# Kernel optimization log

Hardware: AMD Instinct MI355X
Metric: run time of the kernel (lower is better)

Reference implementation:

```python
import jax, jax.numpy as jnp
import numpy as np

N = 4096       # num_nodes (must equal out_features: final div broadcasts [C,N]/[N,1])
IN_F = 1024    # module in_features
OUT_F = 4096   # module out_features == N
F_RAW = 512    # raw node feature dim fed to the in-forward Linear


def setup_inputs() -> dict:
    key = jax.random.key(0)
    ks = jax.random.split(key, 5)
    node_features = jax.random.normal(ks[0], (N, F_RAW), dtype=jnp.float32)
    adjacency_matrix = jax.random.bernoulli(ks[1], 0.004, (N, N)).astype(jnp.float32)
    eye = jnp.eye(N, dtype=jnp.float32)
    A0 = adjacency_matrix * (1.0 - eye)                 # adjacency w/o self loops
    S = (A0 @ A0 + A0) * (1.0 - eye)                    # sibling matrix, zero diag
    mask_hadamard = S[:, None, :]                       # [N,1,N]
    mask_father = adjacency_matrix[:, None, :]          # [N,1,N]
    neighbor_count = jnp.maximum(A0.sum(axis=1, keepdims=True), 1.0)  # [N,1]
    lim = float(1.0 / np.sqrt(F_RAW))
    linear_w = jax.random.uniform(ks[2], (IN_F, F_RAW), minval=-lim, maxval=lim, dtype=jnp.float32)
    linear_b = jax.random.uniform(ks[3], (IN_F,), minval=-lim, maxval=lim, dtype=jnp.float32)
    weight = jax.random.normal(ks[4], (IN_F, OUT_F), dtype=jnp.float32) * float(np.sqrt(2.0 / IN_F))
    return dict(node_features=node_features, adjacency_matrix=adjacency_matrix,
                mask_father=mask_father, neighbor_count=neighbor_count,
                mask_hadamard=mask_hadamard, linear_w=linear_w, linear_b=linear_b,
                weight=weight)


def reference(node_features, adjacency_matrix, mask_father, neighbor_count,
              mask_hadamard, linear_w, linear_b, weight):
    # Linear + projection: wf[n,c]
    x = node_features @ linear_w.T + linear_b           # [N, IN_F]
    wf = x @ weight                                      # [N, C]
    # Original builds masked_hadamard[j,i,c] = wf[i,c]*wf[j,c]*S[i,j] ([N,C,N]),
    # contracts with adjacency over i, masks with adj[k,j], sums over k:
    #   sum_hadamard[c,j] = wf[j,c] * sum_i (sum_k adj[k,j]*adj[k,i]) * S[i,j] * wf[i,c]
    # Fused form avoids the O(N^2 C) intermediates; same math.
    A_out = mask_father[:, 0, :]                         # adj[k,j]  [N,N]
    S = mask_hadamard[:, 0, :]                           # S[i,j]    [N,N]
    G = A_out.T @ adjacency_matrix                       # G[j,i] = sum_k adj[k,j]*adj[k,i]
    P = G * S.T                                          # P[j,i] = G[j,i]*S[i,j]
    sum_hadamard = (wf * (P @ wf)).T                     # [C, N]
    # Final broadcast division exactly as torch: [C,N] / [N,1] (requires C==N)
    return sum_hadamard / jnp.square(neighbor_count)
```

## Files before the change

kernel.cpp:

```cpp
#include <hip/hip_runtime.h>
#include <hip/hip_bf16.h>

typedef __attribute__((ext_vector_type(8))) short s16x8;
typedef __attribute__((ext_vector_type(4))) float f32x4;
typedef __attribute__((ext_vector_type(8))) unsigned short u16x8;

__device__ __forceinline__ float b2f(unsigned short u) {
  union { unsigned int i; float f; } x; x.i = ((unsigned int)u) << 16; return x.f;
}
__device__ __forceinline__ unsigned short f2b(float f) {
  __hip_bfloat16 h = __float2bfloat16(f);
  return *reinterpret_cast<unsigned short*>(&h);
}

#define TILE 128
#define BK 32
#define PCAP 128
#define SCAP 1024

template <int EPI>
__global__ __launch_bounds__(256) void gemm_nt(
    const unsigned short* __restrict__ A,
    const unsigned short* __restrict__ B,
    unsigned short* __restrict__ C,
    int M, int N, int K,
    const float* __restrict__ epi_f)
{
  __shared__ unsigned short As[2][TILE * BK];
  __shared__ unsigned short Bs[2][TILE * BK];
  const int tid  = threadIdx.x;
  const int lane = tid & 63;
  const int wave = tid >> 6;
  const int wm = (wave & 1) * 64;
  const int wn = (wave >> 1) * 64;
  const long bm = (long)blockIdx.y * TILE;
  const long bn = (long)blockIdx.x * TILE;

  f32x4 acc[4][4] = {};

  auto STAGE = [&](int kt, int b) {
    const long kb = (long)kt * BK;
#pragma unroll
    for (int i = 0; i < 2; ++i) {
      const int c0 = (wave * 2 + i) * 64;
      const int c  = c0 + lane;
      const int r  = c >> 2;
      const int cc = ((c & 3) ^ ((c >> 3) & 3)) * 8;
      const unsigned short* ga = A + (bm + r) * (long)K + kb + cc;
      const unsigned short* gb = B + (bn + r) * (long)K + kb + cc;
      __builtin_amdgcn_global_load_lds(
          (const __attribute__((address_space(1))) void*)ga,
          (__attribute__((address_space(3))) void*)(&As[b][c0 * 8]), 16, 0, 0);
      __builtin_amdgcn_global_load_lds(
          (const __attribute__((address_space(1))) void*)gb,
          (__attribute__((address_space(3))) void*)(&Bs[b][c0 * 8]), 16, 0, 0);
    }
  };

  const int kTiles = K / BK;
  STAGE(0, 0);

  for (int kt = 0; kt < kTiles; ++kt) {
    const int cur = kt & 1;
    if (kt + 1 < kTiles) {
      STAGE(kt + 1, cur ^ 1);
      asm volatile("s_waitcnt vmcnt(4)" ::: "memory");
    } else {
      asm volatile("s_waitcnt vmcnt(0)" ::: "memory");
    }
    __builtin_amdgcn_sched_barrier(0);
    __builtin_amdgcn_s_barrier();
    __builtin_amdgcn_sched_barrier(0);

    const int rl = lane & 15;
    const int kqx = ((lane >> 4) ^ ((rl >> 1) & 3)) * 8;
    s16x8 af[4], bfr[4];
#pragma unroll
    for (int mi = 0; mi < 4; ++mi)
      af[mi] = *(const s16x8*)(&As[cur][(wm + mi * 16 + rl) * BK + kqx]);
#pragma unroll
    for (int ni = 0; ni < 4; ++ni)
      bfr[ni] = *(const s16x8*)(&Bs[cur][(wn + ni * 16 + rl) * BK + kqx]);
#pragma unroll
    for (int mi = 0; mi < 4; ++mi)
#pragma unroll
      for (int ni = 0; ni < 4; ++ni)
        acc[mi][ni] = __builtin_amdgcn_mfma_f32_16x16x32_bf16(af[mi], bfr[ni], acc[mi][ni], 0, 0, 0);

    __builtin_amdgcn_sched_barrier(0);
    __builtin_amdgcn_s_barrier();
    __builtin_amdgcn_sched_barrier(0);
  }

  const int cl = lane & 15;
  const int rq = (lane >> 4) * 4;
#pragma unroll
  for (int mi = 0; mi < 4; ++mi)
#pragma unroll
    for (int ni = 0; ni < 4; ++ni)
#pragma unroll
      for (int r = 0; r < 4; ++r) {
        const long row = bm + wm + mi * 16 + rq + r;
        const long col = bn + wn + ni * 16 + cl;
        float v = acc[mi][ni][r];
        if (EPI == 1) v += epi_f[col];
        C[row * (long)N + col] = f2b(v);
      }
}

__global__ __launch_bounds__(256) void transpose_f2b(
    const float* __restrict__ in, unsigned short* __restrict__ out, int R, int C)
{
  __shared__ unsigned short tile[64][66];
  const int t = threadIdx.x;
  const long r0 = (long)blockIdx.y * 64;
  const long c0 = (long)blockIdx.x * 64;
#pragma unroll
  for (int i = 0; i < 4; ++i) {
    int v = t + i * 256;
    int r = v >> 4;
    int c = (v & 15) * 4;
    float4 d = *(const float4*)(in + (r0 + r) * (long)C + c0 + c);
    tile[r][c + 0] = f2b(d.x); tile[r][c + 1] = f2b(d.y);
    tile[r][c + 2] = f2b(d.z); tile[r][c + 3] = f2b(d.w);
  }
  __syncthreads();
#pragma unroll
  for (int i = 0; i < 4; ++i) {
    int v = t + i * 256;
    int r = v >> 4;
    int c = (v & 15) * 4;
    ushort4 d;
    d.x = tile[c + 0][r]; d.y = tile[c + 1][r]; d.z = tile[c + 2][r]; d.w = tile[c + 3][r];
    *(ushort4*)(out + (c0 + r) * (long)R + r0 + c) = d;
  }
}

__global__ __launch_bounds__(256) void conv_f2b(
    const float* __restrict__ in, unsigned short* __restrict__ out)
{
  const long e = ((long)blockIdx.x * 256 + threadIdx.x) * 4;
  float4 d = *(const float4*)(in + e);
  ushort4 o;
  o.x = f2b(d.x); o.y = f2b(d.y); o.z = f2b(d.z); o.w = f2b(d.w);
  *(ushort4*)(out + e) = o;
}

__global__ __launch_bounds__(256) void zero_f4(float* __restrict__ p)
{
  const long e = ((long)blockIdx.x * 256 + threadIdx.x) * 4;
  *(float4*)(p + e) = make_float4(0.f, 0.f, 0.f, 0.f);
}

__global__ __launch_bounds__(256) void build_colbits(
    const float* __restrict__ adj, unsigned long long* __restrict__ colb)
{
  const int i = blockIdx.x;
  const int t = threadIdx.x;
  const unsigned long long bit = 1ull << (i & 63);
  const int w = i >> 6;
  const float* r = adj + (long)i * 4096;
#pragma unroll
  for (int q = 0; q < 4; ++q) {
    int c = (t + q * 256) * 4;
    float4 v = *(const float4*)(r + c);
    if (v.x != 0.f) atomicOr(&colb[(long)(c + 0) * 64 + w], bit);
    if (v.y != 0.f) atomicOr(&colb[(long)(c + 1) * 64 + w], bit);
    if (v.z != 0.f) atomicOr(&colb[(long)(c + 2) * 64 + w], bit);
    if (v.w != 0.f) atomicOr(&colb[(long)(c + 3) * 64 + w], bit);
  }
}

__global__ __launch_bounds__(256) void build_P2(
    const float* __restrict__ S, const unsigned long long* __restrict__ colb,
    int* __restrict__ pk, float* __restrict__ pv, int* __restrict__ pcnt)
{
  const int k = blockIdx.x;
  const int t = threadIdx.x;
  const int lane = t & 63;
  __shared__ __align__(16) unsigned long long ck[64];
  __shared__ int jl[SCAP];
  __shared__ float sl[SCAP];
  __shared__ int m;
  if (t == 0) m = 0;
  if (t < 64) ck[t] = colb[(long)k * 64 + t];
  __syncthreads();
  const float* Sr = S + (long)k * 4096;
  const unsigned long long lmask = (1ull << lane) - 1ull;
#pragma unroll
  for (int q = 0; q < 4; ++q) {
    int c = (t + q * 256) * 4;
    float4 v = *(const float4*)(Sr + c);
    float vals[4] = { v.x, v.y, v.z, v.w };
#pragma unroll
    for (int r = 0; r < 4; ++r) {
      float vv = vals[r];
      unsigned long long mask = __ballot(vv != 0.f);
      if (mask) {
        int base;
        if (lane == 0) base = atomicAdd(&m, __popcll(mask));
        base = __shfl(base, 0, 64);
        if (vv != 0.f) {
          int pos = base + __popcll(mask & lmask);
          if (pos < SCAP) { jl[pos] = c + r; sl[pos] = vv; }
        }
      }
    }
  }
  __syncthreads();
  const int mm = min(m, SCAP);
  const int l = t & 7;
  for (int idx = (t >> 3); idx < mm; idx += 32) {
    const int j = jl[idx];
    const ulonglong2* cj = (const ulonglong2*)(colb + (long)j * 64);
    int cnt = 0;
#pragma unroll
    for (int it = 0; it < 4; ++it) {
      ulonglong2 q  = cj[it * 8 + l];
      ulonglong2 cc = *(const ulonglong2*)&ck[it * 16 + l * 2];
      cnt += __popcll(q.x & cc.x) + __popcll(q.y & cc.y);
    }
    cnt += __shfl_down(cnt, 4, 8);
    cnt += __shfl_down(cnt, 2, 8);
    cnt += __shfl_down(cnt, 1, 8);
    if (l == 0 && cnt > 0) {
      int slot = atomicAdd(&pcnt[j], 1);
      if (slot < PCAP) {
        pk[(long)j * PCAP + slot] = k;
        pv[(long)j * PCAP + slot] = (float)cnt * sl[idx];
      }
    }
  }
}

__global__ __launch_bounds__(256) void spmm_fused(
    const int* __restrict__ pk, const float* __restrict__ pv,
    const int* __restrict__ pcnt, const unsigned short* __restrict__ wf,
    const float* __restrict__ nc, float* __restrict__ VO)
{
  __shared__ int   k_l[4][PCAP];
  __shared__ float v_l[4][PCAP];
  __shared__ int   n_s[4];
  const int t = threadIdx.x;
  const int wave = t >> 6;
  const int lane = t & 63;
  const int seg = blockIdx.x;
  const int jb  = blockIdx.y * 4;
  {
    int e0 = t;
    k_l[e0 >> 7][e0 & 127] = pk[(long)(jb + (e0 >> 7)) * PCAP + (e0 & 127)];
    v_l[e0 >> 7][e0 & 127] = pv[(long)(jb + (e0 >> 7)) * PCAP + (e0 & 127)];
    int e1 = t + 256;
    k_l[e1 >> 7][e1 & 127] = pk[(long)(jb + (e1 >> 7)) * PCAP + (e1 & 127)];
    v_l[e1 >> 7][e1 & 127] = pv[(long)(jb + (e1 >> 7)) * PCAP + (e1 & 127)];
    if (t < 4) n_s[t] = min(pcnt[jb + t], PCAP);
  }
  __syncthreads();
  const int j = jb + wave;
  const int n = n_s[wave];
  const int* __restrict__ kk = k_l[wave];
  const float* __restrict__ vv = v_l[wave];
  const int c0 = seg * 512 + lane * 8;

  float acc[8] = {};
  int m = 0;
  for (; m + 8 <= n; m += 8) {
    float vs[8];
    u16x8 d[8];
#pragma unroll
    for (int r = 0; r < 8; ++r) {
      vs[r] = vv[m + r];
      d[r] = *(const u16x8*)(wf + (unsigned)(kk[m + r] * 4096 + c0));
    }
    __builtin_amdgcn_sched_barrier(0);
#pragma unroll
    for (int r = 0; r < 8; ++r)
#pragma unroll
      for (int q = 0; q < 8; ++q)
        acc[q] += vs[r] * b2f(d[r][q]);
  }
  for (; m + 2 <= n; m += 2) {
    const float v0 = vv[m], v1 = vv[m + 1];
    u16x8 a = *(const u16x8*)(wf + (unsigned)(kk[m]     * 4096 + c0));
    u16x8 b = *(const u16x8*)(wf + (unsigned)(kk[m + 1] * 4096 + c0));
#pragma unroll
    for (int q = 0; q < 8; ++q) acc[q] += v0 * b2f(a[q]) + v1 * b2f(b[q]);
  }
  for (; m < n; ++m) {
    const float va = vv[m];
    u16x8 a = *(const u16x8*)(wf + (unsigned)(kk[m] * 4096 + c0));
#pragma unroll
    for (int q = 0; q < 8; ++q) acc[q] += va * b2f(a[q]);
  }
  u16x8 wa = *(const u16x8*)(wf + (unsigned)(j * 4096 + c0));
  float out[8];
#pragma unroll
  for (int q = 0; q < 8; q += 4) {
    float4 nv = *(const float4*)(nc + c0 + q);
    float n4[4] = { nv.x, nv.y, nv.z, nv.w };
#pragma unroll
    for (int r = 0; r < 4; ++r)
      out[q + r] = acc[q + r] * b2f(wa[q + r]) / (n4[r] * n4[r]);
  }
  float* dst = VO + (long)j * 4096 + c0;
  *(float4*)(dst + 0) = make_float4(out[0], out[1], out[2], out[3]);
  *(float4*)(dst + 4) = make_float4(out[4], out[5], out[6], out[7]);
}

__global__ __launch_bounds__(256) void final_transpose(float* __restrict__ D)
{
  const int bx = blockIdx.x, by = blockIdx.y;
  if (by > bx) return;
  const int X = bx * 64, Y = by * 64;
  const bool diag = (bx == by);
  __shared__ float t1[64][65];
  __shared__ float t2[64][65];
  const int t = threadIdx.x;
  const int r0 = t >> 4;
  const int c4 = (t & 15) * 4;
#pragma unroll
  for (int i = 0; i < 4; ++i) {
    int r = r0 + i * 16;
    float4 d = *(const float4*)&D[(long)(Y + r) * 4096 + X + c4];
    t1[r][c4 + 0] = d.x; t1[r][c4 + 1] = d.y; t1[r][c4 + 2] = d.z; t1[r][c4 + 3] = d.w;
    if (!diag) {
      float4 e = *(const float4*)&D[(long)(X + r) * 4096 + Y + c4];
      t2[r][c4 + 0] = e.x; t2[r][c4 + 1] = e.y; t2[r][c4 + 2] = e.z; t2[r][c4 + 3] = e.w;
    }
  }
  __syncthreads();
#pragma unroll
  for (int i = 0; i < 4; ++i) {
    int r = r0 + i * 16;
    float4 o;
    o.x = t1[c4 + 0][r]; o.y = t1[c4 + 1][r]; o.z = t1[c4 + 2][r]; o.w = t1[c4 + 3][r];
    *(float4*)&D[(long)(X + r) * 4096 + Y + c4] = o;
    if (!diag) {
      float4 p;
      p.x = t2[c4 + 0][r]; p.y = t2[c4 + 1][r]; p.z = t2[c4 + 2][r]; p.w = t2[c4 + 3][r];
      *(float4*)&D[(long)(Y + r) * 4096 + X + c4] = p;
    }
  }
}

extern "C" void kernel_launch(void* const* d_in, const int* in_sizes, int n_in,
                              void* d_out, int out_size, void* d_ws, size_t ws_size,
                              hipStream_t stream) {
  const float* nf  = (const float*)d_in[0];
  const float* adj = (const float*)d_in[1];
  const float* nc  = (const float*)d_in[3];
  const float* S   = (const float*)d_in[4];
  const float* lw  = (const float*)d_in[5];
  const float* lb  = (const float*)d_in[6];
  const float* w   = (const float*)d_in[7];

  const int NN = 4096, INF = 1024, FR = 512;
  char* ws = (char*)d_ws;
  unsigned short*      wf      = (unsigned short*)(ws);
  unsigned long long*  colb    = (unsigned long long*)(ws + (32ll << 20));
  int*                 pcnt    = (int*)(ws + (34ll << 20));
  int*                 pk      = (int*)(ws + (35ll << 20));
  float*               pv      = (float*)(ws + (37ll << 20));
  unsigned short*      weightT = (unsigned short*)(ws + (40ll << 20));
  unsigned short*      nfb     = (unsigned short*)(ws + (48ll << 20));
  unsigned short*      lwb     = (unsigned short*)(ws + (52ll << 20));
  unsigned short*      x       = (unsigned short*)(ws + (54ll << 20));
  float*               VO      = (float*)d_out;

  zero_f4<<<516, 256, 0, stream>>>((float*)colb);
  build_colbits<<<NN, 256, 0, stream>>>(adj, colb);
  build_P2<<<NN, 256, 0, stream>>>(S, colb, pk, pv, pcnt);

  transpose_f2b<<<dim3(NN / 64, INF / 64), 256, 0, stream>>>(w, weightT, INF, NN);
  conv_f2b<<<(NN * (long)FR / 4) / 256, 256, 0, stream>>>(nf, nfb);
  conv_f2b<<<(INF * (long)FR / 4) / 256, 256, 0, stream>>>(lw, lwb);
  gemm_nt<1><<<dim3(INF / TILE, NN / TILE), 256, 0, stream>>>(nfb, lwb, x, NN, INF, FR, lb);
  gemm_nt<0><<<dim3(NN / TILE, NN / TILE), 256, 0, stream>>>(x, weightT, wf, NN, NN, INF, nullptr);

  spmm_fused<<<dim3(8, NN / 4), 256, 0, stream>>>(pk, pv, pcnt, wf, nc, VO);

  final_transpose<<<dim3(NN / 64, NN / 64), 256, 0, stream>>>(VO);
}
```

Measured before the change: 387.2 us.

## Merge independent prep, GEMM and sparse-build kernels into heterogeneous fused launches

```diff
diff --git a/kernel.cpp b/kernel.cpp
--- a/kernel.cpp
+++ b/kernel.cpp
@@ -19,22 +19,22 @@
 #define SCAP 1024
 
 template <int EPI>
-__global__ __launch_bounds__(256) void gemm_nt(
+__device__ __forceinline__ void gemm_body(
+    unsigned short* As, unsigned short* Bs,
+    int bx, int by,
     const unsigned short* __restrict__ A,
     const unsigned short* __restrict__ B,
     unsigned short* __restrict__ C,
     int M, int N, int K,
     const float* __restrict__ epi_f)
 {
-  __shared__ unsigned short As[2][TILE * BK];
-  __shared__ unsigned short Bs[2][TILE * BK];
   const int tid  = threadIdx.x;
   const int lane = tid & 63;
   const int wave = tid >> 6;
   const int wm = (wave & 1) * 64;
   const int wn = (wave >> 1) * 64;
-  const long bm = (long)blockIdx.y * TILE;
-  const long bn = (long)blockIdx.x * TILE;
+  const long bm = (long)by * TILE;
+  const long bn = (long)bx * TILE;
 
   f32x4 acc[4][4] = {};
 
@@ -50,10 +50,10 @@
       const unsigned short* gb = B + (bn + r) * (long)K + kb + cc;
       __builtin_amdgcn_global_load_lds(
           (const __attribute__((address_space(1))) void*)ga,
-          (__attribute__((address_space(3))) void*)(&As[b][c0 * 8]), 16, 0, 0);
+          (__attribute__((address_space(3))) void*)(As + b * (TILE * BK) + c0 * 8), 16, 0, 0);
       __builtin_amdgcn_global_load_lds(
           (const __attribute__((address_space(1))) void*)gb,
-          (__attribute__((address_space(3))) void*)(&Bs[b][c0 * 8]), 16, 0, 0);
+          (__attribute__((address_space(3))) void*)(Bs + b * (TILE * BK) + c0 * 8), 16, 0, 0);
     }
   };
 
@@ -77,10 +77,10 @@
     s16x8 af[4], bfr[4];
 #pragma unroll
     for (int mi = 0; mi < 4; ++mi)
-      af[mi] = *(const s16x8*)(&As[cur][(wm + mi * 16 + rl) * BK + kqx]);
+      af[mi] = *(const s16x8*)(As + cur * (TILE * BK) + (wm + mi * 16 + rl) * BK + kqx);
 #pragma unroll
     for (int ni = 0; ni < 4; ++ni)
-      bfr[ni] = *(const s16x8*)(&Bs[cur][(wn + ni * 16 + rl) * BK + kqx]);
+      bfr[ni] = *(const s16x8*)(Bs + cur * (TILE * BK) + (wn + ni * 16 + rl) * BK + kqx);
 #pragma unroll
     for (int mi = 0; mi < 4; ++mi)
 #pragma unroll
@@ -108,54 +108,9 @@
       }
 }
 
-__global__ __launch_bounds__(256) void transpose_f2b(
-    const float* __restrict__ in, unsigned short* __restrict__ out, int R, int C)
-{
-  __shared__ unsigned short tile[64][66];
-  const int t = threadIdx.x;
-  const long r0 = (long)blockIdx.y * 64;
-  const long c0 = (long)blockIdx.x * 64;
-#pragma unroll
-  for (int i = 0; i < 4; ++i) {
-    int v = t + i * 256;
-    int r = v >> 4;
-    int c = (v & 15) * 4;
-    float4 d = *(const float4*)(in + (r0 + r) * (long)C + c0 + c);
-    tile[r][c + 0] = f2b(d.x); tile[r][c + 1] = f2b(d.y);
-    tile[r][c + 2] = f2b(d.z); tile[r][c + 3] = f2b(d.w);
-  }
-  __syncthreads();
-#pragma unroll
-  for (int i = 0; i < 4; ++i) {
-    int v = t + i * 256;
-    int r = v >> 4;
-    int c = (v & 15) * 4;
-    ushort4 d;
-    d.x = tile[c + 0][r]; d.y = tile[c + 1][r]; d.z = tile[c + 2][r]; d.w = tile[c + 3][r];
-    *(ushort4*)(out + (c0 + r) * (long)R + r0 + c) = d;
-  }
-}
-
-__global__ __launch_bounds__(256) void conv_f2b(
-    const float* __restrict__ in, unsigned short* __restrict__ out)
-{
-  const long e = ((long)blockIdx.x * 256 + threadIdx.x) * 4;
-  float4 d = *(const float4*)(in + e);
-  ushort4 o;
-  o.x = f2b(d.x); o.y = f2b(d.y); o.z = f2b(d.z); o.w = f2b(d.w);
-  *(ushort4*)(out + e) = o;
-}
-
-__global__ __launch_bounds__(256) void zero_f4(float* __restrict__ p)
-{
-  const long e = ((long)blockIdx.x * 256 + threadIdx.x) * 4;
-  *(float4*)(p + e) = make_float4(0.f, 0.f, 0.f, 0.f);
-}
-
-__global__ __launch_bounds__(256) void build_colbits(
-    const float* __restrict__ adj, unsigned long long* __restrict__ colb)
-{
-  const int i = blockIdx.x;
+__device__ __forceinline__ void colbits_body(
+    int i, const float* __restrict__ adj, unsigned long long* __restrict__ colb)
+{
   const int t = threadIdx.x;
   const unsigned long long bit = 1ull << (i & 63);
   const int w = i >> 6;
@@ -171,18 +126,18 @@
   }
 }
 
-__global__ __launch_bounds__(256) void build_P2(
+__device__ __forceinline__ void p2_body(
+    char* smem, int k,
     const float* __restrict__ S, const unsigned long long* __restrict__ colb,
     int* __restrict__ pk, float* __restrict__ pv, int* __restrict__ pcnt)
 {
-  const int k = blockIdx.x;
+  unsigned long long* ck = (unsigned long long*)smem;
+  int*   jl = (int*)(smem + 512);
+  float* sl = (float*)(smem + 512 + SCAP * 4);
+  int*   msh = (int*)(smem + 512 + SCAP * 8);
   const int t = threadIdx.x;
   const int lane = t & 63;
-  __shared__ __align__(16) unsigned long long ck[64];
-  __shared__ int jl[SCAP];
-  __shared__ float sl[SCAP];
-  __shared__ int m;
-  if (t == 0) m = 0;
+  if (t == 0) *msh = 0;
   if (t < 64) ck[t] = colb[(long)k * 64 + t];
   __syncthreads();
   const float* Sr = S + (long)k * 4096;
@@ -198,7 +153,7 @@
       unsigned long long mask = __ballot(vv != 0.f);
       if (mask) {
         int base;
-        if (lane == 0) base = atomicAdd(&m, __popcll(mask));
+        if (lane == 0) base = atomicAdd(msh, __popcll(mask));
         base = __shfl(base, 0, 64);
         if (vv != 0.f) {
           int pos = base + __popcll(mask & lmask);
@@ -208,7 +163,7 @@
     }
   }
   __syncthreads();
-  const int mm = min(m, SCAP);
+  const int mm = min(*msh, SCAP);
   const int l = t & 7;
   for (int idx = (t >> 3); idx < mm; idx += 32) {
     const int j = jl[idx];
@@ -230,6 +185,89 @@
         pv[(long)j * PCAP + slot] = (float)cnt * sl[idx];
       }
     }
+  }
+}
+
+__global__ __launch_bounds__(256) void prep_fused(
+    const float* __restrict__ w,  unsigned short* __restrict__ weightT,
+    const float* __restrict__ nf, unsigned short* __restrict__ nfb,
+    const float* __restrict__ lw, unsigned short* __restrict__ lwb,
+    float* __restrict__ zp)
+{
+  __shared__ unsigned short tile[64][66];
+  const int b = blockIdx.x;
+  const int t = threadIdx.x;
+  if (b < 1024) {
+    const int R = 1024, C = 4096;
+    const long r0 = (long)(b >> 6) * 64;
+    const long c0 = (long)(b & 63) * 64;
+#pragma unroll
+    for (int i = 0; i < 4; ++i) {
+      int v = t + i * 256;
+      int r = v >> 4;
+      int c = (v & 15) * 4;
+      float4 d = *(const float4*)(w + (r0 + r) * (long)C + c0 + c);
+      tile[r][c + 0] = f2b(d.x); tile[r][c + 1] = f2b(d.y);
+      tile[r][c + 2] = f2b(d.z); tile[r][c + 3] = f2b(d.w);
+    }
+    __syncthreads();
+#pragma unroll
+    for (int i = 0; i < 4; ++i) {
+      int v = t + i * 256;
+      int r = v >> 4;
+      int c = (v & 15) * 4;
+      ushort4 d;
+      d.x = tile[c + 0][r]; d.y = tile[c + 1][r]; d.z = tile[c + 2][r]; d.w = tile[c + 3][r];
+      *(ushort4*)(weightT + (c0 + r) * (long)R + r0 + c) = d;
+    }
+  } else if (b < 3072) {
+    const long e = ((long)(b - 1024) * 256 + t) * 4;
+    float4 d = *(const float4*)(nf + e);
+    ushort4 o;
+    o.x = f2b(d.x); o.y = f2b(d.y); o.z = f2b(d.z); o.w = f2b(d.w);
+    *(ushort4*)(nfb + e) = o;
+  } else if (b < 3584) {
+    const long e = ((long)(b - 3072) * 256 + t) * 4;
+    float4 d = *(const float4*)(lw + e);
+    ushort4 o;
+    o.x = f2b(d.x); o.y = f2b(d.y); o.z = f2b(d.z); o.w = f2b(d.w);
+    *(ushort4*)(lwb + e) = o;
+  } else {
+    const long e = ((long)(b - 3584) * 256 + t) * 4;
+    *(float4*)(zp + e) = make_float4(0.f, 0.f, 0.f, 0.f);
+  }
+}
+
+__global__ __launch_bounds__(256) void g1_colbits(
+    const unsigned short* __restrict__ nfb, const unsigned short* __restrict__ lwb,
+    unsigned short* __restrict__ x, const float* __restrict__ lb,
+    const float* __restrict__ adj, unsigned long long* __restrict__ colb)
+{
+  extern __shared__ ulonglong2 dsm[];
+  const int b = blockIdx.x;
+  if (b < 256) {
+    unsigned short* As = (unsigned short*)dsm;
+    unsigned short* Bs = As + 2 * TILE * BK;
+    gemm_body<1>(As, Bs, b & 7, b >> 3, nfb, lwb, x, 4096, 1024, 512, lb);
+  } else {
+    colbits_body(b - 256, adj, colb);
+  }
+}
+
+__global__ __launch_bounds__(256) void g0_p2(
+    const unsigned short* __restrict__ x, const unsigned short* __restrict__ weightT,
+    unsigned short* __restrict__ wf,
+    const float* __restrict__ S, const unsigned long long* __restrict__ colb,
+    int* __restrict__ pk, float* __restrict__ pv, int* __restrict__ pcnt)
+{
+  extern __shared__ ulonglong2 dsm[];
+  const int b = blockIdx.x;
+  if (b < 1024) {
+    unsigned short* As = (unsigned short*)dsm;
+    unsigned short* Bs = As + 2 * TILE * BK;
+    gemm_body<0>(As, Bs, b & 31, b >> 5, x, weightT, wf, 4096, 4096, 1024, nullptr);
+  } else {
+    p2_body((char*)dsm, b - 1024, S, colb, pk, pv, pcnt);
   }
 }
 
@@ -354,7 +392,6 @@
   const float* lb  = (const float*)d_in[6];
   const float* w   = (const float*)d_in[7];
 
-  const int NN = 4096, INF = 1024, FR = 512;
   char* ws = (char*)d_ws;
   unsigned short*      wf      = (unsigned short*)(ws);
   unsigned long long*  colb    = (unsigned long long*)(ws + (32ll << 20));
@@ -367,17 +404,9 @@
   unsigned short*      x       = (unsigned short*)(ws + (54ll << 20));
   float*               VO      = (float*)d_out;
 
-  zero_f4<<<516, 256, 0, stream>>>((float*)colb);
-  build_colbits<<<NN, 256, 0, stream>>>(adj, colb);
-  build_P2<<<NN, 256, 0, stream>>>(S, colb, pk, pv, pcnt);
-
-  transpose_f2b<<<dim3(NN / 64, INF / 64), 256, 0, stream>>>(w, weightT, INF, NN);
-  conv_f2b<<<(NN * (long)FR / 4) / 256, 256, 0, stream>>>(nf, nfb);
-  conv_f2b<<<(INF * (long)FR / 4) / 256, 256, 0, stream>>>(lw, lwb);
-  gemm_nt<1><<<dim3(INF / TILE, NN / TILE), 256, 0, stream>>>(nfb, lwb, x, NN, INF, FR, lb);
-  gemm_nt<0><<<dim3(NN / TILE, NN / TILE), 256, 0, stream>>>(x, weightT, wf, NN, NN, INF, nullptr);
-
-  spmm_fused<<<dim3(8, NN / 4), 256, 0, stream>>>(pk, pv, pcnt, wf, nc, VO);
-
-  final_transpose<<<dim3(NN / 64, NN / 64), 256, 0, stream>>>(VO);
-}
+  prep_fused<<<4100, 256, 0, stream>>>(w, weightT, nf, nfb, lw, lwb, (float*)colb);
+  g1_colbits<<<4352, 256, 32768, stream>>>(nfb, lwb, x, lb, adj, colb);
+  g0_p2<<<5120, 256, 32768, stream>>>(x, weightT, wf, S, colb, pk, pv, pcnt);
+  spmm_fused<<<dim3(8, 1024), 256, 0, stream>>>(pk, pv, pcnt, wf, nc, VO);
+  final_transpose<<<dim3(64, 64), 256, 0, stream>>>(VO);
+}
```

Measured after the change: 381.2 us. About the same (-1.6%).
